# Performance work log

Hardware: AMD Instinct MI355X
Metric: run time of the kernel (lower is better)

## Reference

```python
import jax, jax.numpy as jnp
import numpy as np

T, B, IN, H = 512, 4096, 1, 12

def setup_inputs() -> dict:
    key = jax.random.key(0)
    ks = jax.random.split(key, 7)
    s = 1.0 / np.sqrt(H)
    return {
        "X": jax.random.normal(ks[0], (T, B, IN), dtype=jnp.float32),
        "W_ih": jax.random.uniform(ks[1], (4 * H, IN), minval=-s, maxval=s, dtype=jnp.float32),
        "W_hh": jax.random.uniform(ks[2], (4 * H, H), minval=-s, maxval=s, dtype=jnp.float32),
        "b_ih": jax.random.uniform(ks[3], (4 * H,), minval=-s, maxval=s, dtype=jnp.float32),
        "b_hh": jax.random.uniform(ks[4], (4 * H,), minval=-s, maxval=s, dtype=jnp.float32),
        "fc_w": jax.random.uniform(ks[5], (1, H), minval=-s, maxval=s, dtype=jnp.float32),
        "fc_b": jax.random.uniform(ks[6], (1,), minval=-s, maxval=s, dtype=jnp.float32),
    }

def reference(X, W_ih, W_hh, b_ih, b_hh, fc_w, fc_b):
    # Precompute input contribution for all timesteps: [T, B, 4H]
    x_proj = jnp.einsum('tbi,gi->tbg', X, W_ih) + b_ih + b_hh
    h0 = jnp.zeros((X.shape[1], H), dtype=X.dtype)
    c0 = jnp.zeros_like(h0)

    def step(carry, xp_t):
        h, c = carry
        gates = xp_t + h @ W_hh.T  # [B, 4H]
        i, f, g, o = jnp.split(gates, 4, axis=-1)  # PyTorch gate order i,f,g,o
        i = jax.nn.sigmoid(i)
        f = jax.nn.sigmoid(f)
        g = jnp.tanh(g)
        o = jax.nn.sigmoid(o)
        c_new = f * c + i * g
        h_new = o * jnp.tanh(c_new)
        return (h_new, c_new), h_new

    _, hs = jax.lax.scan(step, (h0, c0), x_proj)  # hs: [T, B, H]
    return jnp.einsum('tbh,oh->tbo', hs, fc_w) + fc_b  # [T, B, 1]
```

## Files before the change

kernel.cpp:

```cpp
#include <hip/hip_runtime.h>


#define TT    512
#define NB    4096
#define HH    12
#define RPW   4
#define CHUNK 64
#define XPAD  68
#define HSTR  20

typedef float v2f __attribute__((ext_vector_type(2)));
typedef float v4f __attribute__((ext_vector_type(4)));

static __device__ __forceinline__ v2f pkfma(v2f a, v2f b, v2f c) {
#if __has_builtin(__builtin_elementwise_fma)
    return __builtin_elementwise_fma(a, b, c);
#else
    v2f r; r.x = fmaf(a.x, b.x, c.x); r.y = fmaf(a.y, b.y, c.y); return r;
#endif
}

#define SNEG   (-1.44269504088896340736f)
#define SPOS   ( 2.88539008177792681472f)
#define M2SPOS (-5.77078016355585362944f)

__global__ __launch_bounds__(64, 1)
void lstm_fused(const float* __restrict__ X,
                const float* __restrict__ W_ih,
                const float* __restrict__ W_hh,
                const float* __restrict__ b_ih,
                const float* __restrict__ b_hh,
                const float* __restrict__ fc_w,
                const float* __restrict__ fc_b,
                float* __restrict__ out)
{
    __shared__ __align__(16) float xchunk[RPW][XPAD];
    __shared__ __align__(16) float hsh[RPW][HSTR];

    const int lane = threadIdx.x;
    const int row  = lane >> 4;
    const int j    = lane & 15;
    const int cellbase = blockIdx.x * RPW;
    const int cell = cellbase + row;

    const int jc = (j < HH) ? j : (HH - 1);

    v2f wI[6], wF[6], wG[6], wO[6], fcv[6];
    #pragma unroll
    for (int k = 0; k < 6; ++k) {
        const float* r0 = W_hh + (0 * HH + jc) * HH + 2 * k;
        const float* r1 = W_hh + (1 * HH + jc) * HH + 2 * k;
        const float* r2 = W_hh + (2 * HH + jc) * HH + 2 * k;
        const float* r3 = W_hh + (3 * HH + jc) * HH + 2 * k;
        wI[k].x = SNEG * r0[0];  wI[k].y = SNEG * r0[1];
        wF[k].x = SNEG * r1[0];  wF[k].y = SNEG * r1[1];
        wG[k].x = SPOS * r2[0];  wG[k].y = SPOS * r2[1];
        wO[k].x = SNEG * r3[0];  wO[k].y = SNEG * r3[1];
        fcv[k].x = fc_w[2 * k];  fcv[k].y = fc_w[2 * k + 1];
    }
    v2f wxI, wxF, wxG, wxO, bI, bF, bG, bO, bFC;
    wxI.x = SNEG * W_ih[0 * HH + jc];  wxI.y = 0.0f;
    wxF.x = SNEG * W_ih[1 * HH + jc];  wxF.y = 0.0f;
    wxG.x = SPOS * W_ih[2 * HH + jc];  wxG.y = 0.0f;
    wxO.x = SNEG * W_ih[3 * HH + jc];  wxO.y = 0.0f;
    bI.x = SNEG * (b_ih[0 * HH + jc] + b_hh[0 * HH + jc]);  bI.y = 0.0f;
    bF.x = SNEG * (b_ih[1 * HH + jc] + b_hh[1 * HH + jc]);  bF.y = 0.0f;
    bG.x = SPOS * (b_ih[2 * HH + jc] + b_hh[2 * HH + jc]);  bG.y = 0.0f;
    bO.x = SNEG * (b_ih[3 * HH + jc] + b_hh[3 * HH + jc]);  bO.y = 0.0f;
    bFC.x = fc_b[0];  bFC.y = 0.0f;

    float c2 = 0.0f;
    float hn = 0.0f;

    float* const hrow = &hsh[row][0];
    const int wslot = j;

    unsigned offPrev = 0;
    float* const outp = out + cell;

    hrow[wslot] = 0.0f;
    __builtin_amdgcn_wave_barrier();

    float4 gq = *(const float4*)(X + (size_t)lane * NB + cellbase);

    for (int tc = 0; tc < TT; tc += CHUNK) {
        xchunk[0][lane] = gq.x;
        xchunk[1][lane] = gq.y;
        xchunk[2][lane] = gq.z;
        xchunk[3][lane] = gq.w;
        if (tc + CHUNK < TT)
            gq = *(const float4*)(X + (size_t)(tc + CHUNK + lane) * NB + cellbase);

        float4 xq_next = *(const float4*)&xchunk[row][0];

        for (int t4 = 0; t4 < CHUNK; t4 += 4) {
            const float4 xq = xq_next;
            const int nx = (t4 + 4 < CHUNK) ? (t4 + 4) : t4;
            xq_next = *(const float4*)&xchunk[row][nx];
            const float xs[4] = {xq.x, xq.y, xq.z, xq.w};

            #pragma unroll
            for (int u = 0; u < 4; ++u) {
                const v4f ha = *(const v4f*)&hrow[0];
                const v4f hb = *(const v4f*)&hrow[4];
                const v4f hc = *(const v4f*)&hrow[8];
                v2f hp0; hp0.x = ha.x; hp0.y = ha.y;
                v2f hp1; hp1.x = ha.z; hp1.y = ha.w;
                v2f hp2; hp2.x = hb.x; hp2.y = hb.y;
                v2f hp3; hp3.x = hb.z; hp3.y = hb.w;
                v2f hp4; hp4.x = hc.x; hp4.y = hc.y;
                v2f hp5; hp5.x = hc.z; hp5.y = hc.w;

                v2f xvv; xvv.x = xs[u]; xvv.y = xs[u];
                v2f aI = pkfma(xvv, wxI, bI);
                v2f aF = pkfma(xvv, wxF, bF);
                v2f aG = pkfma(xvv, wxG, bG);
                v2f aO = pkfma(xvv, wxO, bO);
                v2f pf = pkfma(fcv[0], hp0, bFC);
                aI = pkfma(wI[0], hp0, aI);  aF = pkfma(wF[0], hp0, aF);
                aG = pkfma(wG[0], hp0, aG);  aO = pkfma(wO[0], hp0, aO);
                aI = pkfma(wI[1], hp1, aI);  aF = pkfma(wF[1], hp1, aF);
                aG = pkfma(wG[1], hp1, aG);  aO = pkfma(wO[1], hp1, aO);
                pf = pkfma(fcv[1], hp1, pf);
                aI = pkfma(wI[2], hp2, aI);  aF = pkfma(wF[2], hp2, aF);
                aG = pkfma(wG[2], hp2, aG);  aO = pkfma(wO[2], hp2, aO);
                pf = pkfma(fcv[2], hp2, pf);
                aI = pkfma(wI[3], hp3, aI);  aF = pkfma(wF[3], hp3, aF);
                aG = pkfma(wG[3], hp3, aG);  aO = pkfma(wO[3], hp3, aO);
                pf = pkfma(fcv[3], hp3, pf);
                aI = pkfma(wI[4], hp4, aI);  aF = pkfma(wF[4], hp4, aF);
                aG = pkfma(wG[4], hp4, aG);  aO = pkfma(wO[4], hp4, aO);
                pf = pkfma(fcv[4], hp4, pf);
                aI = pkfma(wI[5], hp5, aI);  aF = pkfma(wF[5], hp5, aF);
                aG = pkfma(wG[5], hp5, aG);  aO = pkfma(wO[5], hp5, aO);
                pf = pkfma(fcv[5], hp5, pf);

                const float gi = aI.x + aI.y;
                const float gf = aF.x + aF.y;
                const float gg = aG.x + aG.y;
                const float go = aO.x + aO.y;

                const float Ei = __builtin_amdgcn_exp2f(gi);
                const float Ef = __builtin_amdgcn_exp2f(gf);
                const float Eg = __builtin_amdgcn_exp2f(gg);
                const float Eo = __builtin_amdgcn_exp2f(go);

                const float p = pf.x + pf.y;
                if (j == 0) *(float*)((char*)outp + offPrev) = p;

                const float si = __builtin_amdgcn_rcpf(1.0f + Ei);
                const float sf = __builtin_amdgcn_rcpf(1.0f + Ef);
                const float rg = __builtin_amdgcn_rcpf(1.0f + Eg);
                const float so = __builtin_amdgcn_rcpf(1.0f + Eo);

                const float tgS = fmaf(M2SPOS, rg, SPOS);
                c2 = fmaf(sf, c2, si * tgS);
                const float Ec = __builtin_amdgcn_exp2f(c2);
                const float rc = __builtin_amdgcn_rcpf(1.0f + Ec);
                const float m2so = -2.0f * so;
                hn = fmaf(m2so, rc, so);

                hrow[wslot] = hn;
                __builtin_amdgcn_wave_barrier();

                offPrev = (unsigned)(tc + t4 + u) << 14;
            }
        }
    }

    {
        const v4f ha = *(const v4f*)&hrow[0];
        const v4f hb = *(const v4f*)&hrow[4];
        const v4f hc = *(const v4f*)&hrow[8];
        v2f hp0; hp0.x = ha.x; hp0.y = ha.y;
        v2f hp1; hp1.x = ha.z; hp1.y = ha.w;
        v2f hp2; hp2.x = hb.x; hp2.y = hb.y;
        v2f hp3; hp3.x = hb.z; hp3.y = hb.w;
        v2f hp4; hp4.x = hc.x; hp4.y = hc.y;
        v2f hp5; hp5.x = hc.z; hp5.y = hc.w;
        v2f pf = pkfma(fcv[0], hp0, bFC);
        pf = pkfma(fcv[1], hp1, pf);
        pf = pkfma(fcv[2], hp2, pf);
        pf = pkfma(fcv[3], hp3, pf);
        pf = pkfma(fcv[4], hp4, pf);
        pf = pkfma(fcv[5], hp5, pf);
        const float p = pf.x + pf.y;
        if (j == 0) *(float*)((char*)outp + offPrev) = p;
    }
}

extern "C" void kernel_launch(void* const* d_in, const int* in_sizes, int n_in,
                              void* d_out, int out_size, void* d_ws, size_t ws_size,
                              hipStream_t stream) {
    const float* X    = (const float*)d_in[0];
    const float* W_ih = (const float*)d_in[1];
    const float* W_hh = (const float*)d_in[2];
    const float* b_ih = (const float*)d_in[3];
    const float* b_hh = (const float*)d_in[4];
    const float* fc_w = (const float*)d_in[5];
    const float* fc_b = (const float*)d_in[6];
    float* out = (float*)d_out;

    const int grid = NB / RPW;
    lstm_fused<<<grid, 64, 0, stream>>>(X, W_ih, W_hh, b_ih, b_hh, fc_w, fc_b, out);
}
```

Before: 176.6 us.

## Split LSTM gates across two half-waves per cell and exchange via ds_swizzle

Each wave now handles two batch cells instead of four. Each 16-lane half computes two of the four gates (i/f or g/o) instead of one lane computing all four, and the partner gate values are exchanged with a ds_swizzle XOR-16. This cuts the per-lane FMA chain and transcendental count on the serial recurrence critical path. In exchange it launches twice as many blocks, adds a cross-lane swizzle per step and raises occupancy to 2 per SIMD. Total work per cell is duplicated across more lanes.

```diff
diff --git a/kernel.cpp b/kernel.cpp
--- a/kernel.cpp
+++ b/kernel.cpp
@@ -4,7 +4,7 @@
 #define TT    512
 #define NB    4096
 #define HH    12
-#define RPW   4
+#define RPW   2
 #define CHUNK 64
 #define XPAD  68
 #define HSTR  20
@@ -19,12 +19,15 @@
     v2f r; r.x = fmaf(a.x, b.x, c.x); r.y = fmaf(a.y, b.y, c.y); return r;
 #endif
 }
+static __device__ __forceinline__ v2f splat2(float s) { v2f r; r.x = s; r.y = s; return r; }
 
 #define SNEG   (-1.44269504088896340736f)
 #define SPOS   ( 2.88539008177792681472f)
 #define M2SPOS (-5.77078016355585362944f)
 
-__global__ __launch_bounds__(64, 1)
+#define SWZ_XOR16 0x401F
+
+__global__ __launch_bounds__(64, 2)
 void lstm_fused(const float* __restrict__ X,
                 const float* __restrict__ W_ih,
                 const float* __restrict__ W_hh,
@@ -38,65 +41,62 @@
     __shared__ __align__(16) float hsh[RPW][HSTR];
 
     const int lane = threadIdx.x;
-    const int row  = lane >> 4;
+    const int cell = lane >> 5;
+    const int half = (lane >> 4) & 1;
     const int j    = lane & 15;
     const int cellbase = blockIdx.x * RPW;
-    const int cell = cellbase + row;
-
-    const int jc = (j < HH) ? j : (HH - 1);
-
-    v2f wI[6], wF[6], wG[6], wO[6], fcv[6];
+    const int gcell = cellbase + cell;
+
+    const int jr = (j < HH) ? j : (HH - 1);
+
+    const int   gA = (half ? 2 : 0) * HH + jr;
+    const int   gB = (half ? 3 : 1) * HH + jr;
+    const float sA = half ? SPOS : SNEG;
+    const float* WA = W_hh + gA * HH;
+    const float* WB = W_hh + gB * HH;
+    v2f wK[12];
     #pragma unroll
-    for (int k = 0; k < 6; ++k) {
-        const float* r0 = W_hh + (0 * HH + jc) * HH + 2 * k;
-        const float* r1 = W_hh + (1 * HH + jc) * HH + 2 * k;
-        const float* r2 = W_hh + (2 * HH + jc) * HH + 2 * k;
-        const float* r3 = W_hh + (3 * HH + jc) * HH + 2 * k;
-        wI[k].x = SNEG * r0[0];  wI[k].y = SNEG * r0[1];
-        wF[k].x = SNEG * r1[0];  wF[k].y = SNEG * r1[1];
-        wG[k].x = SPOS * r2[0];  wG[k].y = SPOS * r2[1];
-        wO[k].x = SNEG * r3[0];  wO[k].y = SNEG * r3[1];
-        fcv[k].x = fc_w[2 * k];  fcv[k].y = fc_w[2 * k + 1];
+    for (int k = 0; k < 12; ++k) {
+        wK[k].x = sA   * WA[k];
+        wK[k].y = SNEG * WB[k];
     }
-    v2f wxI, wxF, wxG, wxO, bI, bF, bG, bO, bFC;
-    wxI.x = SNEG * W_ih[0 * HH + jc];  wxI.y = 0.0f;
-    wxF.x = SNEG * W_ih[1 * HH + jc];  wxF.y = 0.0f;
-    wxG.x = SPOS * W_ih[2 * HH + jc];  wxG.y = 0.0f;
-    wxO.x = SNEG * W_ih[3 * HH + jc];  wxO.y = 0.0f;
-    bI.x = SNEG * (b_ih[0 * HH + jc] + b_hh[0 * HH + jc]);  bI.y = 0.0f;
-    bF.x = SNEG * (b_ih[1 * HH + jc] + b_hh[1 * HH + jc]);  bF.y = 0.0f;
-    bG.x = SPOS * (b_ih[2 * HH + jc] + b_hh[2 * HH + jc]);  bG.y = 0.0f;
-    bO.x = SNEG * (b_ih[3 * HH + jc] + b_hh[3 * HH + jc]);  bO.y = 0.0f;
-    bFC.x = fc_b[0];  bFC.y = 0.0f;
+    v2f wxv, bv;
+    wxv.x = sA   * W_ih[gA];
+    wxv.y = SNEG * W_ih[gB];
+    bv.x  = sA   * (b_ih[gA] + b_hh[gA]);
+    bv.y  = SNEG * (b_ih[gB] + b_hh[gB]);
+
+    v2f fcv[6], bFCv;
+    #pragma unroll
+    for (int k = 0; k < 6; ++k) { fcv[k].x = fc_w[2 * k]; fcv[k].y = fc_w[2 * k + 1]; }
+    bFCv.x = fc_b[0];  bFCv.y = 0.0f;
 
     float c2 = 0.0f;
     float hn = 0.0f;
 
-    float* const hrow = &hsh[row][0];
-    const int wslot = j;
+    float* const hrow = &hsh[cell][0];
 
     unsigned offPrev = 0;
-    float* const outp = out + cell;
-
-    hrow[wslot] = 0.0f;
+    float* const outp = out + gcell;
+
+    if (!half) hrow[j] = 0.0f;
     __builtin_amdgcn_wave_barrier();
 
-    float4 gq = *(const float4*)(X + (size_t)lane * NB + cellbase);
+    float2 gq = *(const float2*)(X + (size_t)lane * NB + cellbase);
 
     for (int tc = 0; tc < TT; tc += CHUNK) {
         xchunk[0][lane] = gq.x;
         xchunk[1][lane] = gq.y;
-        xchunk[2][lane] = gq.z;
-        xchunk[3][lane] = gq.w;
         if (tc + CHUNK < TT)
-            gq = *(const float4*)(X + (size_t)(tc + CHUNK + lane) * NB + cellbase);
-
-        float4 xq_next = *(const float4*)&xchunk[row][0];
+            gq = *(const float2*)(X + (size_t)(tc + CHUNK + lane) * NB + cellbase);
+        __builtin_amdgcn_wave_barrier();
+
+        float4 xq_next = *(const float4*)&xchunk[cell][0];
 
         for (int t4 = 0; t4 < CHUNK; t4 += 4) {
             const float4 xq = xq_next;
             const int nx = (t4 + 4 < CHUNK) ? (t4 + 4) : t4;
-            xq_next = *(const float4*)&xchunk[row][nx];
+            xq_next = *(const float4*)&xchunk[cell][nx];
             const float xs[4] = {xq.x, xq.y, xq.z, xq.w};
 
             #pragma unroll
@@ -104,63 +104,57 @@
                 const v4f ha = *(const v4f*)&hrow[0];
                 const v4f hb = *(const v4f*)&hrow[4];
                 const v4f hc = *(const v4f*)&hrow[8];
+
+                v2f aA = pkfma(splat2(xs[u]), wxv, bv);
+                v2f aB; aB.x = 0.0f; aB.y = 0.0f;
+                aA = pkfma(wK[0],  splat2(ha.x), aA);
+                aB = pkfma(wK[1],  splat2(ha.y), aB);
+                aA = pkfma(wK[2],  splat2(ha.z), aA);
+                aB = pkfma(wK[3],  splat2(ha.w), aB);
+                aA = pkfma(wK[4],  splat2(hb.x), aA);
+                aB = pkfma(wK[5],  splat2(hb.y), aB);
+                aA = pkfma(wK[6],  splat2(hb.z), aA);
+                aB = pkfma(wK[7],  splat2(hb.w), aB);
+                aA = pkfma(wK[8],  splat2(hc.x), aA);
+                aB = pkfma(wK[9],  splat2(hc.y), aB);
+                aA = pkfma(wK[10], splat2(hc.z), aA);
+                aB = pkfma(wK[11], splat2(hc.w), aB);
+                const v2f a = aA + aB;
+
+                const float E0 = __builtin_amdgcn_exp2f(a.x);
+                const float E1 = __builtin_amdgcn_exp2f(a.y);
+
                 v2f hp0; hp0.x = ha.x; hp0.y = ha.y;
                 v2f hp1; hp1.x = ha.z; hp1.y = ha.w;
                 v2f hp2; hp2.x = hb.x; hp2.y = hb.y;
                 v2f hp3; hp3.x = hb.z; hp3.y = hb.w;
                 v2f hp4; hp4.x = hc.x; hp4.y = hc.y;
                 v2f hp5; hp5.x = hc.z; hp5.y = hc.w;
-
-                v2f xvv; xvv.x = xs[u]; xvv.y = xs[u];
-                v2f aI = pkfma(xvv, wxI, bI);
-                v2f aF = pkfma(xvv, wxF, bF);
-                v2f aG = pkfma(xvv, wxG, bG);
-                v2f aO = pkfma(xvv, wxO, bO);
-                v2f pf = pkfma(fcv[0], hp0, bFC);
-                aI = pkfma(wI[0], hp0, aI);  aF = pkfma(wF[0], hp0, aF);
-                aG = pkfma(wG[0], hp0, aG);  aO = pkfma(wO[0], hp0, aO);
-                aI = pkfma(wI[1], hp1, aI);  aF = pkfma(wF[1], hp1, aF);
-                aG = pkfma(wG[1], hp1, aG);  aO = pkfma(wO[1], hp1, aO);
+                v2f pf = pkfma(fcv[0], hp0, bFCv);
                 pf = pkfma(fcv[1], hp1, pf);
-                aI = pkfma(wI[2], hp2, aI);  aF = pkfma(wF[2], hp2, aF);
-                aG = pkfma(wG[2], hp2, aG);  aO = pkfma(wO[2], hp2, aO);
                 pf = pkfma(fcv[2], hp2, pf);
-                aI = pkfma(wI[3], hp3, aI);  aF = pkfma(wF[3], hp3, aF);
-                aG = pkfma(wG[3], hp3, aG);  aO = pkfma(wO[3], hp3, aO);
                 pf = pkfma(fcv[3], hp3, pf);
-                aI = pkfma(wI[4], hp4, aI);  aF = pkfma(wF[4], hp4, aF);
-                aG = pkfma(wG[4], hp4, aG);  aO = pkfma(wO[4], hp4, aO);
                 pf = pkfma(fcv[4], hp4, pf);
-                aI = pkfma(wI[5], hp5, aI);  aF = pkfma(wF[5], hp5, aF);
-                aG = pkfma(wG[5], hp5, aG);  aO = pkfma(wO[5], hp5, aO);
                 pf = pkfma(fcv[5], hp5, pf);
 
-                const float gi = aI.x + aI.y;
-                const float gf = aF.x + aF.y;
-                const float gg = aG.x + aG.y;
-                const float go = aO.x + aO.y;
-
-                const float Ei = __builtin_amdgcn_exp2f(gi);
-                const float Ef = __builtin_amdgcn_exp2f(gf);
-                const float Eg = __builtin_amdgcn_exp2f(gg);
-                const float Eo = __builtin_amdgcn_exp2f(go);
+                const float r0 = __builtin_amdgcn_rcpf(1.0f + E0);
+                const float r1 = __builtin_amdgcn_rcpf(1.0f + E1);
+                const float t0 = fmaf(M2SPOS, r0, SPOS);
+
+                const float x0 = __int_as_float(
+                    __builtin_amdgcn_ds_swizzle(__float_as_int(t0), SWZ_XOR16));
+                const float x1 = __int_as_float(
+                    __builtin_amdgcn_ds_swizzle(__float_as_int(r1), SWZ_XOR16));
 
                 const float p = pf.x + pf.y;
-                if (j == 0) *(float*)((char*)outp + offPrev) = p;
-
-                const float si = __builtin_amdgcn_rcpf(1.0f + Ei);
-                const float sf = __builtin_amdgcn_rcpf(1.0f + Ef);
-                const float rg = __builtin_amdgcn_rcpf(1.0f + Eg);
-                const float so = __builtin_amdgcn_rcpf(1.0f + Eo);
-
-                const float tgS = fmaf(M2SPOS, rg, SPOS);
-                c2 = fmaf(sf, c2, si * tgS);
+                if ((lane & 31) == 0) *(float*)((char*)outp + offPrev) = p;
+
+                c2 = fmaf(r1, c2, r0 * x0);
                 const float Ec = __builtin_amdgcn_exp2f(c2);
                 const float rc = __builtin_amdgcn_rcpf(1.0f + Ec);
-                const float m2so = -2.0f * so;
-                hn = fmaf(m2so, rc, so);
-
-                hrow[wslot] = hn;
+                hn = fmaf(-2.0f * x1, rc, x1);
+
+                if (!half) hrow[j] = hn;
                 __builtin_amdgcn_wave_barrier();
 
                 offPrev = (unsigned)(tc + t4 + u) << 14;
@@ -178,14 +172,14 @@
         v2f hp3; hp3.x = hb.z; hp3.y = hb.w;
         v2f hp4; hp4.x = hc.x; hp4.y = hc.y;
         v2f hp5; hp5.x = hc.z; hp5.y = hc.w;
-        v2f pf = pkfma(fcv[0], hp0, bFC);
+        v2f pf = pkfma(fcv[0], hp0, bFCv);
         pf = pkfma(fcv[1], hp1, pf);
         pf = pkfma(fcv[2], hp2, pf);
         pf = pkfma(fcv[3], hp3, pf);
         pf = pkfma(fcv[4], hp4, pf);
         pf = pkfma(fcv[5], hp5, pf);
         const float p = pf.x + pf.y;
-        if (j == 0) *(float*)((char*)outp + offPrev) = p;
+        if ((lane & 31) == 0) *(float*)((char*)outp + offPrev) = p;
     }
 }
 
```

Result: slower. 191.1 us (+8.2%).
